# Kernel optimization log

Hardware: AMD Instinct MI355X
Metric: run time of the kernel (lower is better)

## Reference

```python
import jax, jax.numpy as jnp
import numpy as np

B, S, HID = 2, 2048, 2048
NH, HD = 16, 128
KVC, QC = 512, 1536


def _rope(x):
    # x: [B, H, S, D]; interleaved-pair rotation matching the torch view(..., D//2, 2)
    b, h, s, d = x.shape
    inv_freq = 1.0 / (10000.0 ** (jnp.arange(0, d, 2, dtype=jnp.float32) / d))  # [D/2]
    pos = jnp.arange(s, dtype=jnp.float32)
    sinusoid = pos[:, None] * inv_freq[None, :]  # [S, D/2]
    sin = jnp.sin(sinusoid)[None, None]  # [1,1,S,D/2]
    cos = jnp.cos(sinusoid)[None, None]
    xr = x.reshape(b, h, s, d // 2, 2)
    x1, x2 = xr[..., 0], xr[..., 1]
    out = jnp.stack([x1 * cos - x2 * sin, x1 * sin + x2 * cos], axis=-1)
    return out.reshape(b, h, s, d)


def setup_inputs() -> dict:
    key = jax.random.key(0)
    ks = jax.random.split(key, 14)
    def lin(k, fan_in, fan_out):
        lim = 1.0 / np.sqrt(fan_in)
        kw, kb = jax.random.split(k)
        W = jax.random.uniform(kw, (fan_in, fan_out), jnp.float32, -lim, lim)
        b = jax.random.uniform(kb, (fan_out,), jnp.float32, -lim, lim)
        return W, b
    x = jax.random.normal(ks[0], (B, S, HID), jnp.float32)
    # causal mask (positions with 0 are masked out)
    attention_mask = jnp.tril(jnp.ones((S, S), jnp.int32))[None, None]  # [1,1,S,S]
    W_dkv, b_dkv = lin(ks[1], HID, KVC)
    W_uk, b_uk = lin(ks[2], KVC, NH * HD)
    W_uv, b_uv = lin(ks[3], KVC, NH * HD)
    W_dq, b_dq = lin(ks[4], HID, QC)
    W_uq, b_uq = lin(ks[5], QC, NH * HD)
    W_o, b_o = lin(ks[6], NH * HD, HID)
    return dict(x=x, attention_mask=attention_mask,
                W_dkv=W_dkv, b_dkv=b_dkv, W_uk=W_uk, b_uk=b_uk,
                W_uv=W_uv, b_uv=b_uv, W_dq=W_dq, b_dq=b_dq,
                W_uq=W_uq, b_uq=b_uq, W_o=W_o, b_o=b_o)


def reference(x, attention_mask, W_dkv, b_dkv, W_uk, b_uk, W_uv, b_uv,
              W_dq, b_dq, W_uq, b_uq, W_o, b_o):
    b, s, _ = x.shape
    kv = x @ W_dkv + b_dkv                                   # [B,S,KVC]
    k = (kv @ W_uk + b_uk).reshape(b, s, NH, HD).transpose(0, 2, 1, 3)  # [B,H,S,D]
    v = (kv @ W_uv + b_uv).reshape(b, s, NH, HD).transpose(0, 2, 1, 3)
    q = ((x @ W_dq + b_dq) @ W_uq + b_uq).reshape(b, s, NH, HD).transpose(0, 2, 1, 3)
    q, k = _rope(q), _rope(k)
    scores = jnp.einsum('bhqd,bhkd->bhqk', q, k) / jnp.sqrt(jnp.float32(HD))
    scores = jnp.where(attention_mask == 0, jnp.float32(-1e9), scores)
    probs = jax.nn.softmax(scores, axis=-1)
    out = jnp.einsum('bhqk,bhkd->bhqd', probs, v)            # [B,H,S,D]
    out = out.transpose(0, 2, 1, 3).reshape(b, s, NH * HD)
    return out @ W_o + b_o
```

## Files before the change

### kernel.cpp

```cpp
#include <hip/hip_runtime.h>
#include <stdint.h>

typedef unsigned short u16;
typedef uint32_t u32;
typedef __attribute__((ext_vector_type(8))) short short8;
typedef __attribute__((ext_vector_type(4))) float f32x4;
typedef __attribute__((ext_vector_type(4))) u32 u32x4;
typedef __attribute__((ext_vector_type(2))) u32 u32x2;
typedef __attribute__((ext_vector_type(4))) unsigned short u16x4;

#define BS_ 4096
#define S_ 2048
#define HID_ 2048
#define KVB 64

__device__ __forceinline__ float bf2f(u16 u) { union { u32 i; float f; } v; v.i = ((u32)u) << 16; return v.f; }
__device__ __forceinline__ u16 f2bf(float f) {
  union { float f; u32 i; } v; v.f = f;
  u32 r = v.i + 0x7fffu + ((v.i >> 16) & 1u);
  return (u16)(r >> 16);
}

__device__ __forceinline__ void gload16(const void* gsrc, void* ldst) {
  __builtin_amdgcn_global_load_lds(
      (const __attribute__((address_space(1))) void*)gsrc,
      (__attribute__((address_space(3))) void*)ldst, 16, 0, 0);
}

__global__ __launch_bounds__(256) void conv_f2b(const float* __restrict__ in, u16* __restrict__ out, int n4) {
  int i = blockIdx.x * 256 + threadIdx.x;
  if (i < n4) {
    float4 v = ((const float4*)in)[i];
    u16x4 o;
    o.x = f2bf(v.x); o.y = f2bf(v.y); o.z = f2bf(v.z); o.w = f2bf(v.w);
    ((u16x4*)out)[i] = o;
  }
}

__global__ __launch_bounds__(256) void transpose_conv(const float* __restrict__ W, u16* __restrict__ WT,
                                                      int K, int N) {
  __shared__ float tile[64][65];
  const int t = threadIdx.x;
  const int kb = blockIdx.y * 64, nb = blockIdx.x * 64;
#pragma unroll
  for (int c = 0; c < 4; ++c) {
    int idx = c * 256 + t;
    int row = idx >> 4;
    int col4 = (idx & 15) * 4;
    float4 v = *(const float4*)&W[(size_t)(kb + row) * N + nb + col4];
    tile[row][col4 + 0] = v.x; tile[row][col4 + 1] = v.y;
    tile[row][col4 + 2] = v.z; tile[row][col4 + 3] = v.w;
  }
  __syncthreads();
#pragma unroll
  for (int c = 0; c < 4; ++c) {
    int idx = c * 256 + t;
    int n = idx >> 4;
    int k4 = (idx & 15) * 4;
    u16x4 o;
    o.x = f2bf(tile[k4 + 0][n]); o.y = f2bf(tile[k4 + 1][n]);
    o.z = f2bf(tile[k4 + 2][n]); o.w = f2bf(tile[k4 + 3][n]);
    *(u16x4*)&WT[(size_t)(nb + n) * K + kb + k4] = o;
  }
}

__global__ __launch_bounds__(256) void concat_bias(const float* __restrict__ b_dkv, const float* __restrict__ b_dq,
                                                   const float* __restrict__ b_uk, const float* __restrict__ b_uv,
                                                   float* __restrict__ bc1, float* __restrict__ bc2) {
  int i = blockIdx.x * 256 + threadIdx.x;
  if (i < 512) bc1[i] = b_dkv[i];
  else if (i < 2048) bc1[i] = b_dq[i - 512];
  else if (i < 4096) bc2[i - 2048] = b_uk[i - 2048];
  else if (i < 6144) bc2[i - 2048] = b_uv[i - 4096];
}

__global__ __launch_bounds__(256) void vtrans(const u16* __restrict__ KVin, u16* __restrict__ VT) {
  __shared__ u16 tile[64][136];
  const int t = threadIdx.x;
  const int st0 = blockIdx.x * 64;
  const int bh = blockIdx.y;
  const int bb = bh >> 4, h = bh & 15;
  const u16* src = KVin + (size_t)bb * S_ * 4096 + 2048 + (size_t)h * 128;
  u16* dst = VT + (size_t)bh * 128 * S_;
#pragma unroll
  for (int c = 0; c < 4; ++c) {
    int idx = c * 256 + t;
    int s = idx >> 4, ch = idx & 15;
    short8 v = *(const short8*)&src[(size_t)(st0 + s) * 4096 + ch * 8];
    *(short8*)&tile[s][ch * 8] = v;
  }
  __syncthreads();
#pragma unroll
  for (int c = 0; c < 4; ++c) {
    int idx = c * 256 + t;
    int d = idx >> 3, ch = idx & 7;
    short8 o;
#pragma unroll
    for (int j = 0; j < 8; ++j) o[j] = tile[ch * 8 + j][d];
    *(short8*)&dst[(size_t)d * S_ + st0 + ch * 8] = o;
  }
}

__global__ __launch_bounds__(256) void rope_table(float* __restrict__ ct, float* __restrict__ st) {
  int idx = blockIdx.x * 256 + threadIdx.x;
  int pos = idx >> 6, i = idx & 63;
  float inv = powf(10000.f, -(float)i / 64.f);
  float a = (float)pos * inv;
  ct[idx] = cosf(a);
  st[idx] = sinf(a);
}

__global__ __launch_bounds__(256) void rope_apply(u32* __restrict__ buf, const float* __restrict__ ct,
                                                  const float* __restrict__ st, int row_stride_pairs) {
  int idx = blockIdx.x * 256 + threadIdx.x;
  int row = idx >> 10, cp = idx & 1023;
  int s = row & 2047;
  int i = cp & 63;
  size_t a = (size_t)row * row_stride_pairs + cp;
  u32 v = buf[a];
  float x1 = bf2f((u16)(v & 0xffff)), x2 = bf2f((u16)(v >> 16));
  float c = ct[s * 64 + i], sn = st[s * 64 + i];
  float o1 = x1 * c - x2 * sn;
  float o2 = x1 * sn + x2 * c;
  buf[a] = (u32)f2bf(o1) | ((u32)f2bf(o2) << 16);
}

template <int OUTF32>
__global__ __launch_bounds__(256) void gemm_bt(const u16* __restrict__ A, int lda,
                                               const u16* __restrict__ BT,
                                               const float* __restrict__ bias, void* __restrict__ Cout,
                                               int M, int N, int K) {
  __shared__ u16 As[128 * 64];
  __shared__ u16 Bs[128 * 64];
  const int t = threadIdx.x;
  const int lane = t & 63, wave = t >> 6;
  const int wm = wave >> 1, wn = wave & 1;
  const int gx = gridDim.x;
  const int nwg = gx * gridDim.y;
  const int flat = blockIdx.y * gx + blockIdx.x;
  const int swz = (flat & 7) * (nwg >> 3) + (flat >> 3);
  const int tn = swz % gx, tm = swz / gx;
  const int r16 = lane & 15, q4 = lane >> 4;

  f32x4 acc[4][4];
#pragma unroll
  for (int m = 0; m < 4; ++m)
#pragma unroll
    for (int n = 0; n < 4; ++n) acc[m][n] = (f32x4){0.f, 0.f, 0.f, 0.f};

  for (int kt = 0; kt < K; kt += 64) {
#pragma unroll
    for (int c = 0; c < 4; ++c) {
      int idx = c * 256 + t;
      int row = idx >> 3, ch = idx & 7;
      gload16(&A[(size_t)(tm * 128 + row) * lda + kt + ch * 8], (char*)As + idx * 16);
      gload16(&BT[(size_t)(tn * 128 + row) * K + kt + ch * 8], (char*)Bs + idx * 16);
    }
    __syncthreads();
#pragma unroll
    for (int kk = 0; kk < 64; kk += 32) {
      short8 af[4], bfv[4];
#pragma unroll
      for (int m = 0; m < 4; ++m)
        af[m] = *(const short8*)&As[(wm * 64 + m * 16 + r16) * 64 + kk + q4 * 8];
#pragma unroll
      for (int n = 0; n < 4; ++n)
        bfv[n] = *(const short8*)&Bs[(wn * 64 + n * 16 + r16) * 64 + kk + q4 * 8];
      __builtin_amdgcn_s_setprio(1);
#pragma unroll
      for (int m = 0; m < 4; ++m)
#pragma unroll
        for (int n = 0; n < 4; ++n)
          acc[m][n] = __builtin_amdgcn_mfma_f32_16x16x32_bf16(bfv[n], af[m], acc[m][n], 0, 0, 0);
      __builtin_amdgcn_s_setprio(0);
    }
    __syncthreads();
  }
#pragma unroll
  for (int n = 0; n < 4; ++n) {
    int gc0 = tn * 128 + wn * 64 + n * 16 + q4 * 4;
    float4 bv4 = *(const float4*)&bias[gc0];
#pragma unroll
    for (int m = 0; m < 4; ++m) {
      int grow = tm * 128 + wm * 64 + m * 16 + r16;
      if (OUTF32) {
        float4 o;
        o.x = acc[m][n][0] + bv4.x; o.y = acc[m][n][1] + bv4.y;
        o.z = acc[m][n][2] + bv4.z; o.w = acc[m][n][3] + bv4.w;
        *(float4*)&((float*)Cout)[(size_t)grow * N + gc0] = o;
      } else {
        u16x4 o;
        o.x = f2bf(acc[m][n][0] + bv4.x); o.y = f2bf(acc[m][n][1] + bv4.y);
        o.z = f2bf(acc[m][n][2] + bv4.z); o.w = f2bf(acc[m][n][3] + bv4.w);
        *(u16x4*)&((u16*)Cout)[(size_t)grow * N + gc0] = o;
      }
    }
  }
}

__global__ __launch_bounds__(256, 2) void attn_kernel(const u16* __restrict__ Q, const u16* __restrict__ K,
                                                      int kld, const u16* __restrict__ VT,
                                                      u16* __restrict__ O) {
  __shared__ u16 Kl[2][KVB * 128];
  __shared__ u16 Vl[2][128 * KVB];
  __shared__ u16 Pl[4][16 * 64];
  const int t = threadIdx.x;
  const int lane = t & 63, w = t >> 6;
  const int r16 = lane & 15, q4 = lane >> 4;
  const int b = blockIdx.x;
  const int xcd = b & 7, u = b >> 3;
  const int p = u & 15, g4 = u >> 4;
  const int bh = g4 * 8 + xcd;
  const int bb = bh >> 4, h = bh & 15;
  const u16* Qb = Q + (size_t)bb * S_ * HID_ + (size_t)h * 128;
  const u16* Kb = K + (size_t)bb * S_ * kld + (size_t)h * 128;
  const u16* VTb = VT + (size_t)bh * 128 * S_;
  u16* Ob = O + (size_t)bb * S_ * HID_ + (size_t)h * 128;

  auto stage = [&](int buf, int kvbase) {
#pragma unroll
    for (int c = 0; c < 4; ++c) {
      int s = c * 256 + t;
      int row = s >> 4;
      int chs = (s & 15) ^ (row & 7);
      gload16(&Kb[(size_t)(kvbase + row) * kld + chs * 8], (char*)Kl[buf] + s * 16);
    }
#pragma unroll
    for (int c = 0; c < 4; ++c) {
      int s = c * 256 + t;
      int row = s >> 3;
      int chs = (s & 7) ^ (row & 7);
      gload16(&VTb[(size_t)row * S_ + kvbase + chs * 8], (char*)Vl[buf] + s * 16);
    }
  };

  u16* Pw = &Pl[w][0];
  const float SCALE = 0.08838834764831845f;

#pragma unroll
  for (int seg = 0; seg < 2; ++seg) {
    const int qt = seg ? (31 - p) : p;
    const int nt = qt + 1;
    const int qrow0 = qt * 64 + w * 16;
    const int q = qrow0 + r16;

    short8 qf[4];
#pragma unroll
    for (int dk = 0; dk < 4; ++dk)
      qf[dk] = *(const short8*)&Qb[(size_t)q * HID_ + dk * 32 + q4 * 8];

    f32x4 ao[8];
#pragma unroll
    for (int dn = 0; dn < 8; ++dn) ao[dn] = (f32x4){0.f, 0.f, 0.f, 0.f};
    float mr = -1e30f, lr = 0.f;

    stage(0, 0);
    __syncthreads();

    for (int ti = 0; ti < nt; ++ti) {
      const int buf = ti & 1;
      const int kv0 = ti * KVB;
      if (ti + 1 < nt) stage(buf ^ 1, kv0 + KVB);

      f32x4 sc[4];
#pragma unroll
      for (int n = 0; n < 4; ++n) sc[n] = (f32x4){0.f, 0.f, 0.f, 0.f};
#pragma unroll
      for (int dk = 0; dk < 4; ++dk) {
        short8 kf[4];
#pragma unroll
        for (int n = 0; n < 4; ++n) {
          int kr = n * 16 + r16;
          int ba = (kr * 256 + dk * 64 + q4 * 16) ^ ((kr & 7) << 4);
          kf[n] = *(const short8*)((const char*)Kl[buf] + ba);
        }
        __builtin_amdgcn_s_setprio(1);
#pragma unroll
        for (int n = 0; n < 4; ++n)
          sc[n] = __builtin_amdgcn_mfma_f32_16x16x32_bf16(kf[n], qf[dk], sc[n], 0, 0, 0);
        __builtin_amdgcn_s_setprio(0);
      }
      const bool nm = (kv0 + 63 > qrow0);
#pragma unroll
      for (int n = 0; n < 4; ++n)
#pragma unroll
        for (int j = 0; j < 4; ++j) {
          float sv = sc[n][j] * SCALE;
          if (nm) {
            int kv = kv0 + n * 16 + q4 * 4 + j;
            if (kv > q) sv = -1e30f;
          }
          sc[n][j] = sv;
        }
      float tm = sc[0][0];
#pragma unroll
      for (int n = 0; n < 4; ++n)
#pragma unroll
        for (int j = 0; j < 4; ++j) tm = fmaxf(tm, sc[n][j]);
      tm = fmaxf(tm, __shfl_xor(tm, 16));
      tm = fmaxf(tm, __shfl_xor(tm, 32));
      if (!__all(tm - mr <= 8.0f)) {
        float mnew = fmaxf(mr, tm);
        float fsc = __expf(mr - mnew);
        lr *= fsc; mr = mnew;
#pragma unroll
        for (int dn = 0; dn < 8; ++dn) ao[dn] *= fsc;
      }
      float ps = 0.f;
#pragma unroll
      for (int n = 0; n < 4; ++n)
#pragma unroll
        for (int j = 0; j < 4; ++j) {
          float pv = __expf(sc[n][j] - mr);
          sc[n][j] = pv;
          ps += pv;
        }
      ps += __shfl_xor(ps, 16);
      ps += __shfl_xor(ps, 32);
      lr += ps;
#pragma unroll
      for (int n = 0; n < 4; ++n) {
        u32 lo, hi;
        asm("v_cvt_pk_bf16_f32 %0, %1, %2" : "=v"(lo) : "v"(sc[n][0]), "v"(sc[n][1]));
        asm("v_cvt_pk_bf16_f32 %0, %1, %2" : "=v"(hi) : "v"(sc[n][2]), "v"(sc[n][3]));
        u32x2 pr; pr.x = lo; pr.y = hi;
        int ba = (r16 * 128 + n * 32 + q4 * 8) ^ ((r16 & 7) << 4);
        *(u32x2*)((char*)Pw + ba) = pr;
      }
#pragma unroll
      for (int s = 0; s < 2; ++s) {
        int bp = (r16 * 128 + s * 64 + q4 * 16) ^ ((r16 & 7) << 4);
        short8 pb = *(const short8*)((const char*)Pw + bp);
        __builtin_amdgcn_s_setprio(1);
#pragma unroll
        for (int dn = 0; dn < 8; ++dn) {
          int dr = dn * 16 + r16;
          int bv = (dr * 128 + s * 64 + q4 * 16) ^ ((dr & 7) << 4);
          short8 vf = *(const short8*)((const char*)Vl[buf] + bv);
          ao[dn] = __builtin_amdgcn_mfma_f32_16x16x32_bf16(vf, pb, ao[dn], 0, 0, 0);
        }
        __builtin_amdgcn_s_setprio(0);
      }
      __syncthreads();
    }

    float inv = 1.f / lr;
#pragma unroll
    for (int dn = 0; dn < 8; ++dn) {
      u16x4 o;
#pragma unroll
      for (int j = 0; j < 4; ++j) o[j] = f2bf(ao[dn][j] * inv);
      *(u16x4*)&Ob[(size_t)q * HID_ + dn * 16 + q4 * 4] = o;
    }
    __syncthreads();
  }
}

extern "C" void kernel_launch(void* const* d_in, const int* in_sizes, int n_in,
                              void* d_out, int out_size, void* d_ws, size_t ws_size,
                              hipStream_t stream) {
  (void)in_sizes; (void)n_in; (void)out_size; (void)ws_size;
  const float* x     = (const float*)d_in[0];
  const float* W_dkv = (const float*)d_in[2];
  const float* b_dkv = (const float*)d_in[3];
  const float* W_uk  = (const float*)d_in[4];
  const float* b_uk  = (const float*)d_in[5];
  const float* W_uv  = (const float*)d_in[6];
  const float* b_uv  = (const float*)d_in[7];
  const float* W_dq  = (const float*)d_in[8];
  const float* b_dq  = (const float*)d_in[9];
  const float* W_uq  = (const float*)d_in[10];
  const float* b_uq  = (const float*)d_in[11];
  const float* W_o   = (const float*)d_in[12];
  const float* b_o   = (const float*)d_in[13];
  float* out = (float*)d_out;

  char* ws = (char*)d_ws;
  size_t off = 0;
  auto carve = [&](size_t bytes) { void* p = ws + off; off += (bytes + 255) & ~(size_t)255; return p; };
  u16* xb     = (u16*)carve((size_t)BS_ * 2048 * 2);
  u16* WdkvqT = (u16*)carve((size_t)2048 * 2048 * 2);
  u16* WukvT  = (u16*)carve((size_t)4096 * 512 * 2);
  u16* WuqT   = (u16*)carve((size_t)2048 * 1536 * 2);
  u16* WoT    = (u16*)carve((size_t)2048 * 2048 * 2);
  u16* kvq1   = (u16*)carve((size_t)BS_ * 2048 * 2);
  u16* kvbuf  = (u16*)carve((size_t)BS_ * 4096 * 2);
  u16* qb     = (u16*)carve((size_t)BS_ * 2048 * 2);
  u16* aob    = (u16*)carve((size_t)BS_ * 2048 * 2);
  float* ct   = (float*)carve((size_t)2048 * 64 * 4);
  float* st   = (float*)carve((size_t)2048 * 64 * 4);
  float* bc1  = (float*)carve((size_t)2048 * 4);
  float* bc2  = (float*)carve((size_t)4096 * 4);
  u16* VT     = xb;

  conv_f2b<<<dim3(BS_ * 2048 / 4 / 256), 256, 0, stream>>>(x, xb, BS_ * 2048 / 4);
  transpose_conv<<<dim3(512 / 64, 2048 / 64), 256, 0, stream>>>(W_dkv, WdkvqT, 2048, 512);
  transpose_conv<<<dim3(1536 / 64, 2048 / 64), 256, 0, stream>>>(W_dq, WdkvqT + (size_t)512 * 2048, 2048, 1536);
  transpose_conv<<<dim3(2048 / 64, 512 / 64), 256, 0, stream>>>(W_uk, WukvT, 512, 2048);
  transpose_conv<<<dim3(2048 / 64, 512 / 64), 256, 0, stream>>>(W_uv, WukvT + (size_t)2048 * 512, 512, 2048);
  transpose_conv<<<dim3(2048 / 64, 1536 / 64), 256, 0, stream>>>(W_uq, WuqT, 1536, 2048);
  transpose_conv<<<dim3(2048 / 64, 2048 / 64), 256, 0, stream>>>(W_o, WoT, 2048, 2048);
  rope_table<<<dim3(512), 256, 0, stream>>>(ct, st);
  concat_bias<<<dim3(24), 256, 0, stream>>>(b_dkv, b_dq, b_uk, b_uv, bc1, bc2);

  gemm_bt<0><<<dim3(2048 / 128, BS_ / 128), 256, 0, stream>>>(xb, 2048, WdkvqT, bc1, kvq1, BS_, 2048, 2048);
  gemm_bt<0><<<dim3(4096 / 128, BS_ / 128), 256, 0, stream>>>(kvq1, 2048, WukvT, bc2, kvbuf, BS_, 4096, 512);
  gemm_bt<0><<<dim3(2048 / 128, BS_ / 128), 256, 0, stream>>>(kvq1 + 512, 2048, WuqT, b_uq, qb, BS_, 2048, 1536);

  rope_apply<<<dim3(BS_ * 1024 / 256), 256, 0, stream>>>((u32*)qb, ct, st, 1024);
  rope_apply<<<dim3(BS_ * 1024 / 256), 256, 0, stream>>>((u32*)kvbuf, ct, st, 2048);
  vtrans<<<dim3(S_ / 64, 32), 256, 0, stream>>>(kvbuf, VT);

  attn_kernel<<<dim3(512), 256, 0, stream>>>(qb, kvbuf, 4096, VT, aob);

  gemm_bt<1><<<dim3(2048 / 128, BS_ / 128), 256, 0, stream>>>(aob, 2048, WoT, b_o, out, BS_, 2048, 2048);
}
```

Measured before the change: 317.0 us.

## Fuse RoPE into GEMM epilogue and halve attention KV tile for higher occupancy

RoPE is now applied in the GEMM epilogue using an interleaved cos/sin table, so the two separate rope_apply passes and their read-modify-write traffic over Q and K are gone. Separately, the attention KV tile shrinks from 64 to 32 rows. The LDS swizzles for V and P are reworked to match, and launch bounds rise to 4 blocks per CU. This trades more loop iterations and barriers, plus smaller MFMA batches per tile, for higher occupancy and latency hiding.

```diff
diff --git a/kernel.cpp b/kernel.cpp
--- a/kernel.cpp
+++ b/kernel.cpp
@@ -12,7 +12,7 @@
 #define BS_ 4096
 #define S_ 2048
 #define HID_ 2048
-#define KVB 64
+#define KVB 32
 
 __device__ __forceinline__ float bf2f(u16 u) { union { u32 i; float f; } v; v.i = ((u32)u) << 16; return v.f; }
 __device__ __forceinline__ u16 f2bf(float f) {
@@ -101,34 +101,21 @@
   }
 }
 
-__global__ __launch_bounds__(256) void rope_table(float* __restrict__ ct, float* __restrict__ st) {
+__global__ __launch_bounds__(256) void rope_table(float* __restrict__ cs) {
   int idx = blockIdx.x * 256 + threadIdx.x;
   int pos = idx >> 6, i = idx & 63;
   float inv = powf(10000.f, -(float)i / 64.f);
   float a = (float)pos * inv;
-  ct[idx] = cosf(a);
-  st[idx] = sinf(a);
-}
-
-__global__ __launch_bounds__(256) void rope_apply(u32* __restrict__ buf, const float* __restrict__ ct,
-                                                  const float* __restrict__ st, int row_stride_pairs) {
-  int idx = blockIdx.x * 256 + threadIdx.x;
-  int row = idx >> 10, cp = idx & 1023;
-  int s = row & 2047;
-  int i = cp & 63;
-  size_t a = (size_t)row * row_stride_pairs + cp;
-  u32 v = buf[a];
-  float x1 = bf2f((u16)(v & 0xffff)), x2 = bf2f((u16)(v >> 16));
-  float c = ct[s * 64 + i], sn = st[s * 64 + i];
-  float o1 = x1 * c - x2 * sn;
-  float o2 = x1 * sn + x2 * c;
-  buf[a] = (u32)f2bf(o1) | ((u32)f2bf(o2) << 16);
-}
-
-template <int OUTF32>
+  cs[idx * 2] = cosf(a);
+  cs[idx * 2 + 1] = sinf(a);
+}
+
+template <int OUTF32, int ROPE>
 __global__ __launch_bounds__(256) void gemm_bt(const u16* __restrict__ A, int lda,
                                                const u16* __restrict__ BT,
-                                               const float* __restrict__ bias, void* __restrict__ Cout,
+                                               const float* __restrict__ bias,
+                                               const float* __restrict__ cs,
+                                               void* __restrict__ Cout,
                                                int M, int N, int K) {
   __shared__ u16 As[128 * 64];
   __shared__ u16 Bs[128 * 64];
@@ -180,30 +167,38 @@
   for (int n = 0; n < 4; ++n) {
     int gc0 = tn * 128 + wn * 64 + n * 16 + q4 * 4;
     float4 bv4 = *(const float4*)&bias[gc0];
+    const int i0 = (gc0 & 127) >> 1;
 #pragma unroll
     for (int m = 0; m < 4; ++m) {
       int grow = tm * 128 + wm * 64 + m * 16 + r16;
+      float v0 = acc[m][n][0] + bv4.x, v1 = acc[m][n][1] + bv4.y;
+      float v2 = acc[m][n][2] + bv4.z, v3 = acc[m][n][3] + bv4.w;
+      if (ROPE && gc0 < ROPE) {
+        int s = grow & 2047;
+        float4 cp = *(const float4*)&cs[((size_t)s * 64 + i0) * 2];
+        float y0 = v0 * cp.x - v1 * cp.y;
+        float y1 = v0 * cp.y + v1 * cp.x;
+        float y2 = v2 * cp.z - v3 * cp.w;
+        float y3 = v2 * cp.w + v3 * cp.z;
+        v0 = y0; v1 = y1; v2 = y2; v3 = y3;
+      }
       if (OUTF32) {
-        float4 o;
-        o.x = acc[m][n][0] + bv4.x; o.y = acc[m][n][1] + bv4.y;
-        o.z = acc[m][n][2] + bv4.z; o.w = acc[m][n][3] + bv4.w;
+        float4 o; o.x = v0; o.y = v1; o.z = v2; o.w = v3;
         *(float4*)&((float*)Cout)[(size_t)grow * N + gc0] = o;
       } else {
-        u16x4 o;
-        o.x = f2bf(acc[m][n][0] + bv4.x); o.y = f2bf(acc[m][n][1] + bv4.y);
-        o.z = f2bf(acc[m][n][2] + bv4.z); o.w = f2bf(acc[m][n][3] + bv4.w);
+        u16x4 o; o.x = f2bf(v0); o.y = f2bf(v1); o.z = f2bf(v2); o.w = f2bf(v3);
         *(u16x4*)&((u16*)Cout)[(size_t)grow * N + gc0] = o;
       }
     }
   }
 }
 
-__global__ __launch_bounds__(256, 2) void attn_kernel(const u16* __restrict__ Q, const u16* __restrict__ K,
+__global__ __launch_bounds__(256, 4) void attn_kernel(const u16* __restrict__ Q, const u16* __restrict__ K,
                                                       int kld, const u16* __restrict__ VT,
                                                       u16* __restrict__ O) {
   __shared__ u16 Kl[2][KVB * 128];
   __shared__ u16 Vl[2][128 * KVB];
-  __shared__ u16 Pl[4][16 * 64];
+  __shared__ u16 Pl[4][16 * KVB];
   const int t = threadIdx.x;
   const int lane = t & 63, w = t >> 6;
   const int r16 = lane & 15, q4 = lane >> 4;
@@ -219,28 +214,29 @@
 
   auto stage = [&](int buf, int kvbase) {
 #pragma unroll
-    for (int c = 0; c < 4; ++c) {
+    for (int c = 0; c < 2; ++c) {
       int s = c * 256 + t;
       int row = s >> 4;
       int chs = (s & 15) ^ (row & 7);
       gload16(&Kb[(size_t)(kvbase + row) * kld + chs * 8], (char*)Kl[buf] + s * 16);
     }
 #pragma unroll
-    for (int c = 0; c < 4; ++c) {
+    for (int c = 0; c < 2; ++c) {
       int s = c * 256 + t;
-      int row = s >> 3;
-      int chs = (s & 7) ^ (row & 7);
+      int row = s >> 2;
+      int chs = (s & 3) ^ ((row >> 1) & 3);
       gload16(&VTb[(size_t)row * S_ + kvbase + chs * 8], (char*)Vl[buf] + s * 16);
     }
   };
 
   u16* Pw = &Pl[w][0];
   const float SCALE = 0.08838834764831845f;
+  const int pswz = (r16 >> 1) & 3;
 
 #pragma unroll
   for (int seg = 0; seg < 2; ++seg) {
     const int qt = seg ? (31 - p) : p;
-    const int nt = qt + 1;
+    const int nt = 2 * qt + 2;
     const int qrow0 = qt * 64 + w * 16;
     const int q = qrow0 + r16;
 
@@ -262,27 +258,26 @@
       const int kv0 = ti * KVB;
       if (ti + 1 < nt) stage(buf ^ 1, kv0 + KVB);
 
-      f32x4 sc[4];
-#pragma unroll
-      for (int n = 0; n < 4; ++n) sc[n] = (f32x4){0.f, 0.f, 0.f, 0.f};
+      f32x4 sc[2];
+      sc[0] = (f32x4){0.f, 0.f, 0.f, 0.f};
+      sc[1] = (f32x4){0.f, 0.f, 0.f, 0.f};
 #pragma unroll
       for (int dk = 0; dk < 4; ++dk) {
-        short8 kf[4];
-#pragma unroll
-        for (int n = 0; n < 4; ++n) {
+        short8 kf[2];
+#pragma unroll
+        for (int n = 0; n < 2; ++n) {
           int kr = n * 16 + r16;
           int ba = (kr * 256 + dk * 64 + q4 * 16) ^ ((kr & 7) << 4);
           kf[n] = *(const short8*)((const char*)Kl[buf] + ba);
         }
         __builtin_amdgcn_s_setprio(1);
-#pragma unroll
-        for (int n = 0; n < 4; ++n)
-          sc[n] = __builtin_amdgcn_mfma_f32_16x16x32_bf16(kf[n], qf[dk], sc[n], 0, 0, 0);
+        sc[0] = __builtin_amdgcn_mfma_f32_16x16x32_bf16(kf[0], qf[dk], sc[0], 0, 0, 0);
+        sc[1] = __builtin_amdgcn_mfma_f32_16x16x32_bf16(kf[1], qf[dk], sc[1], 0, 0, 0);
         __builtin_amdgcn_s_setprio(0);
       }
-      const bool nm = (kv0 + 63 > qrow0);
-#pragma unroll
-      for (int n = 0; n < 4; ++n)
+      const bool nm = (kv0 + 31 > qrow0);
+#pragma unroll
+      for (int n = 0; n < 2; ++n)
 #pragma unroll
         for (int j = 0; j < 4; ++j) {
           float sv = sc[n][j] * SCALE;
@@ -294,7 +289,7 @@
         }
       float tm = sc[0][0];
 #pragma unroll
-      for (int n = 0; n < 4; ++n)
+      for (int n = 0; n < 2; ++n)
 #pragma unroll
         for (int j = 0; j < 4; ++j) tm = fmaxf(tm, sc[n][j]);
       tm = fmaxf(tm, __shfl_xor(tm, 16));
@@ -308,7 +303,7 @@
       }
       float ps = 0.f;
 #pragma unroll
-      for (int n = 0; n < 4; ++n)
+      for (int n = 0; n < 2; ++n)
 #pragma unroll
         for (int j = 0; j < 4; ++j) {
           float pv = __expf(sc[n][j] - mr);
@@ -319,23 +314,23 @@
       ps += __shfl_xor(ps, 32);
       lr += ps;
 #pragma unroll
-      for (int n = 0; n < 4; ++n) {
+      for (int n = 0; n < 2; ++n) {
         u32 lo, hi;
         asm("v_cvt_pk_bf16_f32 %0, %1, %2" : "=v"(lo) : "v"(sc[n][0]), "v"(sc[n][1]));
         asm("v_cvt_pk_bf16_f32 %0, %1, %2" : "=v"(hi) : "v"(sc[n][2]), "v"(sc[n][3]));
         u32x2 pr; pr.x = lo; pr.y = hi;
-        int ba = (r16 * 128 + n * 32 + q4 * 8) ^ ((r16 & 7) << 4);
+        int chunk = (n * 2 + (q4 >> 1)) ^ pswz;
+        int ba = r16 * 64 + chunk * 16 + (q4 & 1) * 8;
         *(u32x2*)((char*)Pw + ba) = pr;
       }
-#pragma unroll
-      for (int s = 0; s < 2; ++s) {
-        int bp = (r16 * 128 + s * 64 + q4 * 16) ^ ((r16 & 7) << 4);
+      {
+        int bp = r16 * 64 + ((q4 ^ pswz) * 16);
         short8 pb = *(const short8*)((const char*)Pw + bp);
         __builtin_amdgcn_s_setprio(1);
 #pragma unroll
         for (int dn = 0; dn < 8; ++dn) {
           int dr = dn * 16 + r16;
-          int bv = (dr * 128 + s * 64 + q4 * 16) ^ ((dr & 7) << 4);
+          int bv = dr * 64 + ((q4 ^ ((dr >> 1) & 3)) * 16);
           short8 vf = *(const short8*)((const char*)Vl[buf] + bv);
           ao[dn] = __builtin_amdgcn_mfma_f32_16x16x32_bf16(vf, pb, ao[dn], 0, 0, 0);
         }
@@ -387,8 +382,7 @@
   u16* kvbuf  = (u16*)carve((size_t)BS_ * 4096 * 2);
   u16* qb     = (u16*)carve((size_t)BS_ * 2048 * 2);
   u16* aob    = (u16*)carve((size_t)BS_ * 2048 * 2);
-  float* ct   = (float*)carve((size_t)2048 * 64 * 4);
-  float* st   = (float*)carve((size_t)2048 * 64 * 4);
+  float* cs   = (float*)carve((size_t)2048 * 64 * 2 * 4);
   float* bc1  = (float*)carve((size_t)2048 * 4);
   float* bc2  = (float*)carve((size_t)4096 * 4);
   u16* VT     = xb;
@@ -400,18 +394,16 @@
   transpose_conv<<<dim3(2048 / 64, 512 / 64), 256, 0, stream>>>(W_uv, WukvT + (size_t)2048 * 512, 512, 2048);
   transpose_conv<<<dim3(2048 / 64, 1536 / 64), 256, 0, stream>>>(W_uq, WuqT, 1536, 2048);
   transpose_conv<<<dim3(2048 / 64, 2048 / 64), 256, 0, stream>>>(W_o, WoT, 2048, 2048);
-  rope_table<<<dim3(512), 256, 0, stream>>>(ct, st);
+  rope_table<<<dim3(512), 256, 0, stream>>>(cs);
   concat_bias<<<dim3(24), 256, 0, stream>>>(b_dkv, b_dq, b_uk, b_uv, bc1, bc2);
 
-  gemm_bt<0><<<dim3(2048 / 128, BS_ / 128), 256, 0, stream>>>(xb, 2048, WdkvqT, bc1, kvq1, BS_, 2048, 2048);
-  gemm_bt<0><<<dim3(4096 / 128, BS_ / 128), 256, 0, stream>>>(kvq1, 2048, WukvT, bc2, kvbuf, BS_, 4096, 512);
-  gemm_bt<0><<<dim3(2048 / 128, BS_ / 128), 256, 0, stream>>>(kvq1 + 512, 2048, WuqT, b_uq, qb, BS_, 2048, 1536);
-
-  rope_apply<<<dim3(BS_ * 1024 / 256), 256, 0, stream>>>((u32*)qb, ct, st, 1024);
-  rope_apply<<<dim3(BS_ * 1024 / 256), 256, 0, stream>>>((u32*)kvbuf, ct, st, 2048);
+  gemm_bt<0, 0><<<dim3(2048 / 128, BS_ / 128), 256, 0, stream>>>(xb, 2048, WdkvqT, bc1, nullptr, kvq1, BS_, 2048, 2048);
+  gemm_bt<0, 2048><<<dim3(4096 / 128, BS_ / 128), 256, 0, stream>>>(kvq1, 2048, WukvT, bc2, cs, kvbuf, BS_, 4096, 512);
+  gemm_bt<0, 2048><<<dim3(2048 / 128, BS_ / 128), 256, 0, stream>>>(kvq1 + 512, 2048, WuqT, b_uq, cs, qb, BS_, 2048, 1536);
+
   vtrans<<<dim3(S_ / 64, 32), 256, 0, stream>>>(kvbuf, VT);
 
   attn_kernel<<<dim3(512), 256, 0, stream>>>(qb, kvbuf, 4096, VT, aob);
 
-  gemm_bt<1><<<dim3(2048 / 128, BS_ / 128), 256, 0, stream>>>(aob, 2048, WoT, b_o, out, BS_, 2048, 2048);
-}
+  gemm_bt<1, 0><<<dim3(2048 / 128, BS_ / 128), 256, 0, stream>>>(aob, 2048, WoT, b_o, nullptr, out, BS_, 2048, 2048);
+}
```

Result: no change. 318.1 us (+0.3%).
